# Kernel optimization log

Hardware: AMD Instinct MI355X
Metric: run time of the kernel (lower is better)

## Reference

```python
import jax, jax.numpy as jnp
import numpy as np

N_NODES = 50000
N_EDGES = 600000


def setup_inputs() -> dict:
    key = jax.random.key(0)
    ks = jax.random.split(key, 8)
    d_in, d_h, d_out = 128, 128, 64
    # Glorot-ish scaled weights
    W1 = jax.random.normal(ks[0], (d_in, d_h), jnp.float32) * (1.0 / np.sqrt(d_in))
    W2 = jax.random.normal(ks[1], (d_h, d_h), jnp.float32) * (1.0 / np.sqrt(d_h))
    W3 = jax.random.normal(ks[2], (d_h, d_out), jnp.float32) * (1.0 / np.sqrt(d_h))
    return {
        "features": jax.random.normal(ks[3], (N_NODES, d_in), jnp.float32),
        "src": jax.random.randint(ks[4], (N_EDGES,), 0, N_NODES, jnp.int32),
        "dst": jax.random.randint(ks[5], (N_EDGES,), 0, N_NODES, jnp.int32),
        "W1": W1, "b1": jnp.zeros((d_h,), jnp.float32),
        "W2": W2, "b2": jnp.zeros((d_h,), jnp.float32),
        "W3": W3, "b3": jnp.zeros((d_out,), jnp.float32),
    }


def _graph_conv(h, src, dst, inv_deg, W, b, activate):
    # DGL GraphConv, norm='right': mean-aggregate in-neighbors, then linear.
    # (D^-1 A h) W == D^-1 A (h W), so aggregate-then-matmul is faithful.
    msgs = h[src]  # [E, d] gather
    agg = jax.ops.segment_sum(msgs, dst, num_segments=N_NODES)  # scatter-add
    rst = agg * inv_deg[:, None]
    out = rst @ W + b
    if activate:
        out = jax.nn.relu(out)
    return out


def reference(features, src, dst, W1, b1, W2, b2, W3, b3):
    # in-degree for right normalization (clamped to >=1 as in DGL)
    deg = jax.ops.segment_sum(jnp.ones_like(dst, dtype=features.dtype), dst,
                              num_segments=N_NODES)
    inv_deg = 1.0 / jnp.maximum(deg, 1.0)
    # dropout is identity in eval mode
    h = _graph_conv(features, src, dst, inv_deg, W1, b1, True)
    h = _graph_conv(h, src, dst, inv_deg, W2, b2, True)
    h = _graph_conv(h, src, dst, inv_deg, W3, b3, False)
    return h
```

## Files before the change

### kernel.cpp

```cpp
#include <hip/hip_runtime.h>
#include <stdint.h>


#define N_NODES 50000
#define N_EDGES 600000
#define SCAN_CHUNK 1024

typedef __attribute__((ext_vector_type(8))) short short8v;
typedef __attribute__((ext_vector_type(4))) float f32x4;


__global__ void count_deg_k(const int* __restrict__ dst, int* __restrict__ deg, int e) {
    int i = blockIdx.x * blockDim.x + threadIdx.x;
    if (i < e) atomicAdd(&deg[dst[i]], 1);
}

__global__ __launch_bounds__(256) void scan_part_k(const int* __restrict__ deg,
                                                   int* __restrict__ blockSums, int n) {
    __shared__ int red[256];
    int t = threadIdx.x;
    int base = blockIdx.x * SCAN_CHUNK + t * 4;
    int s = 0;
#pragma unroll
    for (int k = 0; k < 4; ++k) {
        int i = base + k;
        if (i < n) s += deg[i];
    }
    red[t] = s;
    __syncthreads();
    for (int off = 128; off > 0; off >>= 1) {
        if (t < off) red[t] += red[t + off];
        __syncthreads();
    }
    if (t == 0) blockSums[blockIdx.x] = red[0];
}

__global__ void scan_blocks_k(int* __restrict__ blockSums, int nb,
                              int* __restrict__ offs, int n) {
    if (threadIdx.x == 0 && blockIdx.x == 0) {
        int run = 0;
        for (int i = 0; i < nb; ++i) {
            int v = blockSums[i];
            blockSums[i] = run;
            run += v;
        }
        offs[n] = run;
    }
}

__global__ __launch_bounds__(256) void scan_final_k(const int* __restrict__ deg,
                                                    const int* __restrict__ blockSums,
                                                    int* __restrict__ offs,
                                                    int* __restrict__ cursor,
                                                    float* __restrict__ inv, int n) {
    __shared__ int red[256];
    int t = threadIdx.x;
    int base = blockIdx.x * SCAN_CHUNK + t * 4;
    int v[4];
    int s = 0;
#pragma unroll
    for (int k = 0; k < 4; ++k) {
        int i = base + k;
        v[k] = (i < n) ? deg[i] : 0;
        s += v[k];
    }
    red[t] = s;
    __syncthreads();
    for (int off = 1; off < 256; off <<= 1) {
        int x = (t >= off) ? red[t - off] : 0;
        __syncthreads();
        red[t] += x;
        __syncthreads();
    }
    int run = blockSums[blockIdx.x] + red[t] - s;
#pragma unroll
    for (int k = 0; k < 4; ++k) {
        int i = base + k;
        if (i < n) {
            offs[i] = run;
            cursor[i] = run;
            inv[i] = 1.0f / (float)(v[k] > 0 ? v[k] : 1);
            run += v[k];
        }
    }
}

__global__ void fill_csr_k(const int* __restrict__ src, const int* __restrict__ dst,
                           int* __restrict__ cursor, int* __restrict__ esrc, int e) {
    int i = blockIdx.x * blockDim.x + threadIdx.x;
    if (i < e) {
        int p = atomicAdd(&cursor[dst[i]], 1);
        esrc[p] = src[i];
    }
}


__device__ __forceinline__ void prep_one(const float* __restrict__ W, short* hiF,
                                         short* loF, int NC, int idx) {
    int lane = idx & 63;
    int ks = (idx >> 6) & 3;
    int T = idx >> 8;
    int g = lane >> 4, cl = lane & 15;
    int col = T * 16 + cl;
    short8v h, l;
#pragma unroll
    for (int j = 0; j < 8; ++j) {
        int k = ks * 32 + g * 4 + (j & 3) + ((j >> 2) << 4);
        float w = W[(size_t)k * NC + col];
        unsigned u = __float_as_uint(w);
        h[j] = (short)(u >> 16);
        float res = w - __uint_as_float(u & 0xFFFF0000u);
        l[j] = (short)(__float_as_uint(res) >> 16);
    }
    ((short8v*)hiF)[idx] = h;
    ((short8v*)loF)[idx] = l;
}

__global__ void prep_all_k(const float* __restrict__ W1, const float* __restrict__ W2,
                           const float* __restrict__ W3,
                           short* W1h, short* W1l, short* W2h, short* W2l,
                           short* W3h, short* W3l) {
    int idx = blockIdx.x * 256 + threadIdx.x;
    if (idx < 2048) prep_one(W1, W1h, W1l, 128, idx);
    else if (idx < 4096) prep_one(W2, W2h, W2l, 128, idx - 2048);
    else if (idx < 5120) prep_one(W3, W3h, W3l, 64, idx - 4096);
}


template <bool W3TAIL>
__global__ __launch_bounds__(256, 6) void fused_agg_gemm_k(
    const float* __restrict__ h, const int* __restrict__ offs,
    const int* __restrict__ esrc, const float* __restrict__ inv,
    const short* __restrict__ WhF, const short* __restrict__ WlF,
    const float* __restrict__ bias,
    const short* __restrict__ W3hF, const short* __restrict__ W3lF,
    float* __restrict__ out, int n) {
    __shared__ float rows[16][132];
    int wave = threadIdx.x >> 6;
    int lane = threadIdx.x & 63;
    int rowbase = blockIdx.x * 16;

    {
        int half = lane >> 5;
        int l5 = lane & 31;
        const float4* __restrict__ h4 = (const float4*)h;
#pragma unroll
        for (int it = 0; it < 2; ++it) {
            int r = wave * 4 + it * 2 + half;
            int node = rowbase + r;
            float ax = 0.f, ay = 0.f, az = 0.f, aw = 0.f;
            if (node < n) {
                int beg = offs[node], end = offs[node + 1];
                int j = beg;
                for (; j + 4 <= end; j += 4) {
                    int s0 = esrc[j], s1 = esrc[j + 1];
                    int s2 = esrc[j + 2], s3 = esrc[j + 3];
                    float4 v0 = h4[(size_t)s0 * 32 + l5];
                    float4 v1 = h4[(size_t)s1 * 32 + l5];
                    float4 v2 = h4[(size_t)s2 * 32 + l5];
                    float4 v3 = h4[(size_t)s3 * 32 + l5];
                    ax += (v0.x + v1.x) + (v2.x + v3.x);
                    ay += (v0.y + v1.y) + (v2.y + v3.y);
                    az += (v0.z + v1.z) + (v2.z + v3.z);
                    aw += (v0.w + v1.w) + (v2.w + v3.w);
                }
                for (; j < end; ++j) {
                    float4 v = h4[(size_t)esrc[j] * 32 + l5];
                    ax += v.x; ay += v.y; az += v.z; aw += v.w;
                }
                float sc = inv[node];
                ax *= sc; ay *= sc; az *= sc; aw *= sc;
            }
            float4 r4; r4.x = ax; r4.y = ay; r4.z = az; r4.w = aw;
            *(float4*)&rows[r][l5 * 4] = r4;
        }
    }
    __syncthreads();

    int g = lane >> 4, cl = lane & 15;
    short8v ah[4], al[4];
#pragma unroll
    for (int ks = 0; ks < 4; ++ks) {
        const float* rp = &rows[cl][ks * 32 + g * 4];
        float4 aL = *(const float4*)rp;
        float4 aH = *(const float4*)(rp + 16);
#define SPLIT1(D, J, V)                                                     \
        {                                                                   \
            unsigned u = __float_as_uint(V);                                \
            D##h[ks][J] = (short)(u >> 16);                                 \
            float res = (V) - __uint_as_float(u & 0xFFFF0000u);             \
            D##l[ks][J] = (short)(__float_as_uint(res) >> 16);              \
        }
        SPLIT1(a, 0, aL.x) SPLIT1(a, 1, aL.y) SPLIT1(a, 2, aL.z) SPLIT1(a, 3, aL.w)
        SPLIT1(a, 4, aH.x) SPLIT1(a, 5, aH.y) SPLIT1(a, 6, aH.z) SPLIT1(a, 7, aH.w)
#undef SPLIT1
    }
    if (W3TAIL) __syncthreads();

    f32x4 acc[2];
    acc[0] = (f32x4){0.f, 0.f, 0.f, 0.f};
    acc[1] = (f32x4){0.f, 0.f, 0.f, 0.f};
#pragma unroll
    for (int ks = 0; ks < 4; ++ks) {
#pragma unroll
        for (int t = 0; t < 2; ++t) {
            int tileIdx = wave * 2 + t;
            size_t fo = ((size_t)(tileIdx * 4 + ks) * 64 + lane) * 8;
            short8v bh = *(const short8v*)(WhF + fo);
            short8v bl = *(const short8v*)(WlF + fo);
            acc[t] = __builtin_amdgcn_mfma_f32_16x16x32_bf16(ah[ks], bh, acc[t], 0, 0, 0);
            acc[t] = __builtin_amdgcn_mfma_f32_16x16x32_bf16(al[ks], bh, acc[t], 0, 0, 0);
            acc[t] = __builtin_amdgcn_mfma_f32_16x16x32_bf16(ah[ks], bl, acc[t], 0, 0, 0);
        }
    }

#pragma unroll
    for (int t = 0; t < 2; ++t) {
        int col = (wave * 2 + t) * 16 + cl;
        float bv = bias[col];
#pragma unroll
        for (int r = 0; r < 4; ++r) {
            float v = fmaxf(acc[t][r] + bv, 0.f);
            if (!W3TAIL) {
                int gr = rowbase + g * 4 + r;
                if (gr < n) out[(size_t)gr * 128 + col] = v;
            } else {
                rows[g * 4 + r][col] = v;
            }
        }
    }

    if (W3TAIL) {
        __syncthreads();
        f32x4 acc3 = {0.f, 0.f, 0.f, 0.f};
#pragma unroll
        for (int ks = 0; ks < 4; ++ks) {
            const float* rp = &rows[cl][ks * 32 + g * 4];
            float4 aL = *(const float4*)rp;
            float4 aH = *(const float4*)(rp + 16);
            short8v bh2, bl2;
#define SPLIT1(J, V)                                                        \
            {                                                               \
                unsigned u = __float_as_uint(V);                            \
                bh2[J] = (short)(u >> 16);                                  \
                float res = (V) - __uint_as_float(u & 0xFFFF0000u);         \
                bl2[J] = (short)(__float_as_uint(res) >> 16);               \
            }
            SPLIT1(0, aL.x) SPLIT1(1, aL.y) SPLIT1(2, aL.z) SPLIT1(3, aL.w)
            SPLIT1(4, aH.x) SPLIT1(5, aH.y) SPLIT1(6, aH.z) SPLIT1(7, aH.w)
#undef SPLIT1
            size_t fo = ((size_t)(wave * 4 + ks) * 64 + lane) * 8;
            short8v wh = *(const short8v*)(W3hF + fo);
            short8v wl = *(const short8v*)(W3lF + fo);
            acc3 = __builtin_amdgcn_mfma_f32_16x16x32_bf16(bh2, wh, acc3, 0, 0, 0);
            acc3 = __builtin_amdgcn_mfma_f32_16x16x32_bf16(bl2, wh, acc3, 0, 0, 0);
            acc3 = __builtin_amdgcn_mfma_f32_16x16x32_bf16(bh2, wl, acc3, 0, 0, 0);
        }
        int col3 = wave * 16 + cl;
#pragma unroll
        for (int r = 0; r < 4; ++r) {
            int gr = rowbase + g * 4 + r;
            if (gr < n) out[(size_t)gr * 64 + col3] = acc3[r];
        }
    }
}


__global__ __launch_bounds__(256) void agg64_k(const float* __restrict__ t64,
                                               const int* __restrict__ offs,
                                               const int* __restrict__ esrc,
                                               const float* __restrict__ inv,
                                               const float* __restrict__ bias,
                                               float* __restrict__ out, int n) {
    int gt = blockIdx.x * 256 + threadIdx.x;
    int wv = gt >> 6;
    int q = (threadIdx.x >> 4) & 3;
    int l4 = threadIdx.x & 15;
    int node = wv * 4 + q;
    if (node >= n) return;
    int beg = offs[node], end = offs[node + 1];
    const float4* __restrict__ h4 = (const float4*)t64;
    float4 a = {0.f, 0.f, 0.f, 0.f};
    int j = beg;
    for (; j + 4 <= end; j += 4) {
        int s0 = esrc[j], s1 = esrc[j + 1], s2 = esrc[j + 2], s3 = esrc[j + 3];
        float4 v0 = h4[(size_t)s0 * 16 + l4];
        float4 v1 = h4[(size_t)s1 * 16 + l4];
        float4 v2 = h4[(size_t)s2 * 16 + l4];
        float4 v3 = h4[(size_t)s3 * 16 + l4];
        a.x += (v0.x + v1.x) + (v2.x + v3.x);
        a.y += (v0.y + v1.y) + (v2.y + v3.y);
        a.z += (v0.z + v1.z) + (v2.z + v3.z);
        a.w += (v0.w + v1.w) + (v2.w + v3.w);
    }
    for (; j < end; ++j) {
        float4 v = h4[(size_t)esrc[j] * 16 + l4];
        a.x += v.x; a.y += v.y; a.z += v.z; a.w += v.w;
    }
    float sc = inv[node];
    float4 b = ((const float4*)bias)[l4];
    float4 r;
    r.x = a.x * sc + b.x; r.y = a.y * sc + b.y;
    r.z = a.z * sc + b.z; r.w = a.w * sc + b.w;
    ((float4*)out)[(size_t)node * 16 + l4] = r;
}


extern "C" void kernel_launch(void* const* d_in, const int* in_sizes, int n_in,
                              void* d_out, int out_size, void* d_ws, size_t ws_size,
                              hipStream_t stream) {
    const int N = N_NODES, E = N_EDGES;
    const float* feat = (const float*)d_in[0];
    const int* src = (const int*)d_in[1];
    const int* dst = (const int*)d_in[2];
    const float* W1 = (const float*)d_in[3];
    const float* b1 = (const float*)d_in[4];
    const float* W2 = (const float*)d_in[5];
    const float* b2 = (const float*)d_in[6];
    const float* W3 = (const float*)d_in[7];
    const float* b3 = (const float*)d_in[8];
    float* out = (float*)d_out;

    const int nScanBlocks = (N + SCAN_CHUNK - 1) / SCAN_CHUNK;

    float* B0 = (float*)d_ws;
    float* B1 = B0 + (size_t)N * 128;
    int* deg = (int*)(B1 + (size_t)N * 128);
    float* invd = (float*)(deg + N);
    int* offs = (int*)(invd + N);
    int* cursor = offs + N + 2;
    int* esrc = cursor + N;
    int* blockSums = esrc + E;
    short* W1h = (short*)cursor;
    short* W1l = W1h + 16384;
    short* W2h = W1l + 16384;
    short* W2l = W2h + 16384;
    short* W3h = W2l + 16384;
    short* W3l = W3h + 8192;

    hipMemsetAsync(deg, 0, (size_t)N * sizeof(int), stream);
    count_deg_k<<<(E + 255) / 256, 256, 0, stream>>>(dst, deg, E);
    scan_part_k<<<nScanBlocks, 256, 0, stream>>>(deg, blockSums, N);
    scan_blocks_k<<<1, 64, 0, stream>>>(blockSums, nScanBlocks, offs, N);
    scan_final_k<<<nScanBlocks, 256, 0, stream>>>(deg, blockSums, offs, cursor, invd, N);
    fill_csr_k<<<(E + 255) / 256, 256, 0, stream>>>(src, dst, cursor, esrc, E);

    prep_all_k<<<20, 256, 0, stream>>>(W1, W2, W3, W1h, W1l, W2h, W2l, W3h, W3l);

    const int fusedGrid = (N + 15) / 16;
    const int agg64Grid = (N + 15) / 16;

    fused_agg_gemm_k<false><<<fusedGrid, 256, 0, stream>>>(
        feat, offs, esrc, invd, W1h, W1l, b1, nullptr, nullptr, B1, N);
    fused_agg_gemm_k<true><<<fusedGrid, 256, 0, stream>>>(
        B1, offs, esrc, invd, W2h, W2l, b2, W3h, W3l, B0, N);
    agg64_k<<<agg64Grid, 256, 0, stream>>>(B0, offs, esrc, invd, b3, out, N);
}
```

Measured before the change: 281.0 us.

## Store node features and intermediates as bf16 to halve gather traffic

Features are converted to bf16 in the degree-count kernel, and both intermediate hidden layers and the W3 output are written as bf16. The three aggregation kernels then gather 8-byte uint2 rows instead of 16-byte float4 and widen to fp32 for accumulation. This roughly halves the bytes moved by the random-neighbor gathers, which dominate runtime. CSR fill and weight prep are also merged into one launch. The cost is reduced precision in the stored activations, which may drift from the fp32 reference.

```diff
diff --git a/kernel.cpp b/kernel.cpp
--- a/kernel.cpp
+++ b/kernel.cpp
@@ -5,14 +5,34 @@
 #define N_NODES 50000
 #define N_EDGES 600000
 #define SCAN_CHUNK 1024
+#define FILL_BLOCKS ((N_EDGES + 255) / 256)
 
 typedef __attribute__((ext_vector_type(8))) short short8v;
 typedef __attribute__((ext_vector_type(4))) float f32x4;
 
-
-__global__ void count_deg_k(const int* __restrict__ dst, int* __restrict__ deg, int e) {
-    int i = blockIdx.x * blockDim.x + threadIdx.x;
+__device__ __forceinline__ unsigned short f2bf(float f) {
+    unsigned u = __float_as_uint(f);
+    unsigned r = (u + 0x7fffu + ((u >> 16) & 1u)) >> 16;
+    return (unsigned short)r;
+}
+
+
+__global__ void count_cvt_k(const int* __restrict__ dst, int* __restrict__ deg,
+                            const float* __restrict__ feat, uint4* __restrict__ featB,
+                            int e, int n8) {
+    int i = blockIdx.x * 256 + threadIdx.x;
     if (i < e) atomicAdd(&deg[dst[i]], 1);
+    if (i < n8) {
+        const float4* f4 = (const float4*)feat;
+        float4 a = f4[(size_t)i * 2];
+        float4 b = f4[(size_t)i * 2 + 1];
+        uint4 o;
+        o.x = (unsigned)f2bf(a.x) | ((unsigned)f2bf(a.y) << 16);
+        o.y = (unsigned)f2bf(a.z) | ((unsigned)f2bf(a.w) << 16);
+        o.z = (unsigned)f2bf(b.x) | ((unsigned)f2bf(b.y) << 16);
+        o.w = (unsigned)f2bf(b.z) | ((unsigned)f2bf(b.w) << 16);
+        featB[i] = o;
+    }
 }
 
 __global__ __launch_bounds__(256) void scan_part_k(const int* __restrict__ deg,
@@ -85,15 +105,6 @@
     }
 }
 
-__global__ void fill_csr_k(const int* __restrict__ src, const int* __restrict__ dst,
-                           int* __restrict__ cursor, int* __restrict__ esrc, int e) {
-    int i = blockIdx.x * blockDim.x + threadIdx.x;
-    if (i < e) {
-        int p = atomicAdd(&cursor[dst[i]], 1);
-        esrc[p] = src[i];
-    }
-}
-
 
 __device__ __forceinline__ void prep_one(const float* __restrict__ W, short* hiF,
                                          short* loF, int NC, int idx) {
@@ -116,25 +127,36 @@
     ((short8v*)loF)[idx] = l;
 }
 
-__global__ void prep_all_k(const float* __restrict__ W1, const float* __restrict__ W2,
-                           const float* __restrict__ W3,
-                           short* W1h, short* W1l, short* W2h, short* W2l,
-                           short* W3h, short* W3l) {
-    int idx = blockIdx.x * 256 + threadIdx.x;
-    if (idx < 2048) prep_one(W1, W1h, W1l, 128, idx);
-    else if (idx < 4096) prep_one(W2, W2h, W2l, 128, idx - 2048);
-    else if (idx < 5120) prep_one(W3, W3h, W3l, 64, idx - 4096);
+__global__ void fill_prep_k(const int* __restrict__ src, const int* __restrict__ dst,
+                            int* __restrict__ cursor, int* __restrict__ esrc, int e,
+                            const float* __restrict__ W1, const float* __restrict__ W2,
+                            const float* __restrict__ W3,
+                            short* W1h, short* W1l, short* W2h, short* W2l,
+                            short* W3h, short* W3l) {
+    int b = blockIdx.x;
+    if (b < FILL_BLOCKS) {
+        int i = b * 256 + threadIdx.x;
+        if (i < e) {
+            int p = atomicAdd(&cursor[dst[i]], 1);
+            esrc[p] = src[i];
+        }
+    } else {
+        int idx = (b - FILL_BLOCKS) * 256 + threadIdx.x;
+        if (idx < 2048) prep_one(W1, W1h, W1l, 128, idx);
+        else if (idx < 4096) prep_one(W2, W2h, W2l, 128, idx - 2048);
+        else if (idx < 5120) prep_one(W3, W3h, W3l, 64, idx - 4096);
+    }
 }
 
 
 template <bool W3TAIL>
 __global__ __launch_bounds__(256, 6) void fused_agg_gemm_k(
-    const float* __restrict__ h, const int* __restrict__ offs,
+    const unsigned short* __restrict__ hB, const int* __restrict__ offs,
     const int* __restrict__ esrc, const float* __restrict__ inv,
     const short* __restrict__ WhF, const short* __restrict__ WlF,
     const float* __restrict__ bias,
     const short* __restrict__ W3hF, const short* __restrict__ W3lF,
-    float* __restrict__ out, int n) {
+    unsigned short* __restrict__ outB, int n) {
     __shared__ float rows[16][132];
     int wave = threadIdx.x >> 6;
     int lane = threadIdx.x & 63;
@@ -143,7 +165,7 @@
     {
         int half = lane >> 5;
         int l5 = lane & 31;
-        const float4* __restrict__ h4 = (const float4*)h;
+        const uint2* __restrict__ h2 = (const uint2*)hB;
 #pragma unroll
         for (int it = 0; it < 2; ++it) {
             int r = wave * 4 + it * 2 + half;
@@ -152,22 +174,27 @@
             if (node < n) {
                 int beg = offs[node], end = offs[node + 1];
                 int j = beg;
+#define ACC4(V)                                                             \
+                {                                                           \
+                    ax += __uint_as_float((V).x << 16);                     \
+                    ay += __uint_as_float((V).x & 0xffff0000u);             \
+                    az += __uint_as_float((V).y << 16);                     \
+                    aw += __uint_as_float((V).y & 0xffff0000u);             \
+                }
                 for (; j + 4 <= end; j += 4) {
                     int s0 = esrc[j], s1 = esrc[j + 1];
                     int s2 = esrc[j + 2], s3 = esrc[j + 3];
-                    float4 v0 = h4[(size_t)s0 * 32 + l5];
-                    float4 v1 = h4[(size_t)s1 * 32 + l5];
-                    float4 v2 = h4[(size_t)s2 * 32 + l5];
-                    float4 v3 = h4[(size_t)s3 * 32 + l5];
-                    ax += (v0.x + v1.x) + (v2.x + v3.x);
-                    ay += (v0.y + v1.y) + (v2.y + v3.y);
-                    az += (v0.z + v1.z) + (v2.z + v3.z);
-                    aw += (v0.w + v1.w) + (v2.w + v3.w);
+                    uint2 v0 = h2[(size_t)s0 * 32 + l5];
+                    uint2 v1 = h2[(size_t)s1 * 32 + l5];
+                    uint2 v2 = h2[(size_t)s2 * 32 + l5];
+                    uint2 v3 = h2[(size_t)s3 * 32 + l5];
+                    ACC4(v0) ACC4(v1) ACC4(v2) ACC4(v3)
                 }
                 for (; j < end; ++j) {
-                    float4 v = h4[(size_t)esrc[j] * 32 + l5];
-                    ax += v.x; ay += v.y; az += v.z; aw += v.w;
+                    uint2 v = h2[(size_t)esrc[j] * 32 + l5];
+                    ACC4(v)
                 }
+#undef ACC4
                 float sc = inv[node];
                 ax *= sc; ay *= sc; az *= sc; aw *= sc;
             }
@@ -184,15 +211,15 @@
         const float* rp = &rows[cl][ks * 32 + g * 4];
         float4 aL = *(const float4*)rp;
         float4 aH = *(const float4*)(rp + 16);
-#define SPLIT1(D, J, V)                                                     \
+#define SPLIT1(J, V)                                                        \
         {                                                                   \
             unsigned u = __float_as_uint(V);                                \
-            D##h[ks][J] = (short)(u >> 16);                                 \
+            ah[ks][J] = (short)(u >> 16);                                   \
             float res = (V) - __uint_as_float(u & 0xFFFF0000u);             \
-            D##l[ks][J] = (short)(__float_as_uint(res) >> 16);              \
-        }
-        SPLIT1(a, 0, aL.x) SPLIT1(a, 1, aL.y) SPLIT1(a, 2, aL.z) SPLIT1(a, 3, aL.w)
-        SPLIT1(a, 4, aH.x) SPLIT1(a, 5, aH.y) SPLIT1(a, 6, aH.z) SPLIT1(a, 7, aH.w)
+            al[ks][J] = (short)(__float_as_uint(res) >> 16);                \
+        }
+        SPLIT1(0, aL.x) SPLIT1(1, aL.y) SPLIT1(2, aL.z) SPLIT1(3, aL.w)
+        SPLIT1(4, aH.x) SPLIT1(5, aH.y) SPLIT1(6, aH.z) SPLIT1(7, aH.w)
 #undef SPLIT1
     }
     if (W3TAIL) __syncthreads();
@@ -223,7 +250,7 @@
             float v = fmaxf(acc[t][r] + bv, 0.f);
             if (!W3TAIL) {
                 int gr = rowbase + g * 4 + r;
-                if (gr < n) out[(size_t)gr * 128 + col] = v;
+                if (gr < n) outB[(size_t)gr * 128 + col] = f2bf(v);
             } else {
                 rows[g * 4 + r][col] = v;
             }
@@ -260,13 +287,13 @@
 #pragma unroll
         for (int r = 0; r < 4; ++r) {
             int gr = rowbase + g * 4 + r;
-            if (gr < n) out[(size_t)gr * 64 + col3] = acc3[r];
-        }
-    }
-}
-
-
-__global__ __launch_bounds__(256) void agg64_k(const float* __restrict__ t64,
+            if (gr < n) outB[(size_t)gr * 64 + col3] = f2bf(acc3[r]);
+        }
+    }
+}
+
+
+__global__ __launch_bounds__(256) void agg64_k(const unsigned short* __restrict__ tB,
                                                const int* __restrict__ offs,
                                                const int* __restrict__ esrc,
                                                const float* __restrict__ inv,
@@ -279,29 +306,34 @@
     int node = wv * 4 + q;
     if (node >= n) return;
     int beg = offs[node], end = offs[node + 1];
-    const float4* __restrict__ h4 = (const float4*)t64;
-    float4 a = {0.f, 0.f, 0.f, 0.f};
+    const uint2* __restrict__ t2 = (const uint2*)tB;
+    float ax = 0.f, ay = 0.f, az = 0.f, aw = 0.f;
     int j = beg;
+#define ACC4(V)                                                             \
+    {                                                                       \
+        ax += __uint_as_float((V).x << 16);                                 \
+        ay += __uint_as_float((V).x & 0xffff0000u);                         \
+        az += __uint_as_float((V).y << 16);                                 \
+        aw += __uint_as_float((V).y & 0xffff0000u);                         \
+    }
     for (; j + 4 <= end; j += 4) {
         int s0 = esrc[j], s1 = esrc[j + 1], s2 = esrc[j + 2], s3 = esrc[j + 3];
-        float4 v0 = h4[(size_t)s0 * 16 + l4];
-        float4 v1 = h4[(size_t)s1 * 16 + l4];
-        float4 v2 = h4[(size_t)s2 * 16 + l4];
-        float4 v3 = h4[(size_t)s3 * 16 + l4];
-        a.x += (v0.x + v1.x) + (v2.x + v3.x);
-        a.y += (v0.y + v1.y) + (v2.y + v3.y);
-        a.z += (v0.z + v1.z) + (v2.z + v3.z);
-        a.w += (v0.w + v1.w) + (v2.w + v3.w);
+        uint2 v0 = t2[(size_t)s0 * 16 + l4];
+        uint2 v1 = t2[(size_t)s1 * 16 + l4];
+        uint2 v2 = t2[(size_t)s2 * 16 + l4];
+        uint2 v3 = t2[(size_t)s3 * 16 + l4];
+        ACC4(v0) ACC4(v1) ACC4(v2) ACC4(v3)
     }
     for (; j < end; ++j) {
-        float4 v = h4[(size_t)esrc[j] * 16 + l4];
-        a.x += v.x; a.y += v.y; a.z += v.z; a.w += v.w;
-    }
+        uint2 v = t2[(size_t)esrc[j] * 16 + l4];
+        ACC4(v)
+    }
+#undef ACC4
     float sc = inv[node];
     float4 b = ((const float4*)bias)[l4];
     float4 r;
-    r.x = a.x * sc + b.x; r.y = a.y * sc + b.y;
-    r.z = a.z * sc + b.z; r.w = a.w * sc + b.w;
+    r.x = ax * sc + b.x; r.y = ay * sc + b.y;
+    r.z = az * sc + b.z; r.w = aw * sc + b.w;
     ((float4*)out)[(size_t)node * 16 + l4] = r;
 }
 
@@ -331,28 +363,36 @@
     int* cursor = offs + N + 2;
     int* esrc = cursor + N;
     int* blockSums = esrc + E;
-    short* W1h = (short*)cursor;
+    uintptr_t p = (uintptr_t)(blockSums + 64);
+    p = (p + 15) & ~(uintptr_t)15;
+    unsigned short* featB = (unsigned short*)p;
+    short* W1h = (short*)(featB + (size_t)N * 128);
     short* W1l = W1h + 16384;
     short* W2h = W1l + 16384;
     short* W2l = W2h + 16384;
     short* W3h = W2l + 16384;
     short* W3l = W3h + 8192;
 
+    unsigned short* h1B = (unsigned short*)B1;
+    unsigned short* tB = (unsigned short*)B0;
+
     hipMemsetAsync(deg, 0, (size_t)N * sizeof(int), stream);
-    count_deg_k<<<(E + 255) / 256, 256, 0, stream>>>(dst, deg, E);
+    const int n8 = N * 128 / 8;
+    count_cvt_k<<<(n8 + 255) / 256, 256, 0, stream>>>(dst, deg, feat, (uint4*)featB,
+                                                      E, n8);
     scan_part_k<<<nScanBlocks, 256, 0, stream>>>(deg, blockSums, N);
     scan_blocks_k<<<1, 64, 0, stream>>>(blockSums, nScanBlocks, offs, N);
     scan_final_k<<<nScanBlocks, 256, 0, stream>>>(deg, blockSums, offs, cursor, invd, N);
-    fill_csr_k<<<(E + 255) / 256, 256, 0, stream>>>(src, dst, cursor, esrc, E);
-
-    prep_all_k<<<20, 256, 0, stream>>>(W1, W2, W3, W1h, W1l, W2h, W2l, W3h, W3l);
+    fill_prep_k<<<FILL_BLOCKS + 20, 256, 0, stream>>>(src, dst, cursor, esrc, E,
+                                                      W1, W2, W3, W1h, W1l, W2h, W2l,
+                                                      W3h, W3l);
 
     const int fusedGrid = (N + 15) / 16;
     const int agg64Grid = (N + 15) / 16;
 
     fused_agg_gemm_k<false><<<fusedGrid, 256, 0, stream>>>(
-        feat, offs, esrc, invd, W1h, W1l, b1, nullptr, nullptr, B1, N);
+        featB, offs, esrc, invd, W1h, W1l, b1, nullptr, nullptr, h1B, N);
     fused_agg_gemm_k<true><<<fusedGrid, 256, 0, stream>>>(
-        B1, offs, esrc, invd, W2h, W2l, b2, W3h, W3l, B0, N);
-    agg64_k<<<agg64Grid, 256, 0, stream>>>(B0, offs, esrc, invd, b3, out, N);
-}
+        h1B, offs, esrc, invd, W2h, W2l, b2, W3h, W3l, tB, N);
+    agg64_k<<<agg64Grid, 256, 0, stream>>>(tB, offs, esrc, invd, b3, out, N);
+}
```

Result: faster. 247.9 us (-11.8%).
